# Kernel tuning notes

Measured on AMD Instinct MI355X. Metric: run time of the kernel, lower is better.

Reference implementation:

```python
import jax, jax.numpy as jnp
import numpy as np
import math

HEAD = 4

def _neighbors3x3(t):
    # t: [b, g, d, h, w] -> [b, g, d, 9, h, w], zero-padded 3x3 neighborhoods
    b, g, d, h, w = t.shape
    tp = jnp.pad(t, ((0, 0), (0, 0), (0, 0), (1, 1), (1, 1)))
    # torch.nn.Unfold(kernel_size=3) ordering: kernel positions row-major (dy, dx)
    patches = [tp[:, :, :, dy:dy + h, dx:dx + w] for dy in range(3) for dx in range(3)]
    return jnp.stack(patches, axis=3)


def setup_inputs() -> dict:
    key = jax.random.key(0)
    k1, k2 = jax.random.split(key)
    x = jax.random.normal(k1, (8, 128, 96, 96), dtype=jnp.float32)
    # 1x1 conv weight, no bias: [out=3*out_features, in=in_features]
    W_trans = jax.random.normal(k2, (384, 128), dtype=jnp.float32) * 0.05
    return {"x": x, "W_trans": W_trans}


def reference(x, W_trans):
    b, cin, h, w = x.shape
    # 1x1 conv == channel GEMM
    t = jnp.einsum('bchw,oc->bohw', x, W_trans)  # [b, 3*C, h, w]
    q, k, v = jnp.split(t, 3, axis=1)            # each [b, C, h, w]
    C = q.shape[1]
    d = C // HEAD
    q = q.reshape(b, HEAD, d, h, w)
    k = k.reshape(b, HEAD, d, h, w)
    v = v.reshape(b, HEAD, d, h, w)
    kn = _neighbors3x3(k)  # [b, g, d, 9, h, w]
    vn = _neighbors3x3(v)  # [b, g, d, 9, h, w]
    # att[b,g,n,h,w] = <q[b,g,:,h,w], kn[b,g,:,n,h,w]> / sqrt(d)
    att = jnp.einsum('bgdhw,bgdnhw->bgnhw', q, kn) / math.sqrt(d)
    att = jax.nn.softmax(att, axis=2)
    # dropout p=0.4 is identity in eval mode
    out = jnp.einsum('bgnhw,bgdnhw->bgdhw', att, vn)  # [b, g, d, h, w]
    return out.reshape(b, C, h, w)
```

## Files before the change

### kernel.cpp

```cpp
#include <hip/hip_runtime.h>

#define NB     8
#define CIN    128
#define HEADS  4
#define DHEAD  32
#define HDIM   96
#define WDIM   96
#define HW     9216

#define TH     8
#define TW     16
#define HR     (TH + 2)
#define HC     (TW + 2)
#define HP     (HR * HC)
#define NT     12
#define NPOS   (NT * 16)
#define NPOSP  (NPOS + 1)
#define QP     (TH * TW)

typedef __fp16 f16x2 __attribute__((ext_vector_type(2)));
typedef __fp16 f16x8 __attribute__((ext_vector_type(8)));
typedef float  f32x4 __attribute__((ext_vector_type(4)));

__device__ __forceinline__ unsigned pkh2(float a, float b) {
  f16x2 h = __builtin_amdgcn_cvt_pkrtz(a, b);
  return *(unsigned*)&h;
}
__device__ __forceinline__ float dot2(unsigned a, unsigned b, float c) {
#if __has_builtin(__builtin_amdgcn_fdot2)
  return __builtin_amdgcn_fdot2(*(f16x2*)&a, *(f16x2*)&b, c, false);
#else
  f16x2 ha = *(f16x2*)&a, hb = *(f16x2*)&b;
  c = fmaf((float)ha[0], (float)hb[0], c);
  return fmaf((float)ha[1], (float)hb[1], c);
#endif
}

__global__ __launch_bounds__(256) void wpack_kernel(const float* __restrict__ W,
                                                    uint4* __restrict__ Wf) {
  const int u = blockIdx.x * 256 + threadIdx.x;
  const int lane = u & 63, kb = (u >> 6) & 3, ot = u >> 8;
  const int o = ot * 16 + (lane & 15);
  const int c0 = kb * 32 + (lane >> 4) * 8;
  const float4* w = (const float4*)(W + (size_t)o * CIN + c0);
  float4 w0 = w[0], w1 = w[1];
  uint4 r;
  r.x = pkh2(w0.x, w0.y); r.y = pkh2(w0.z, w0.w);
  r.z = pkh2(w1.x, w1.y); r.w = pkh2(w1.z, w1.w);
  Wf[u] = r;
}

__global__ __launch_bounds__(256) void fused_kernel(const float* __restrict__ x,
                                                    const uint4* __restrict__ Wf,
                                                    float* __restrict__ out) {
  __shared__ uint4 qs[4 * QP];
  __shared__ uint4 ks[4 * NPOSP];
  __shared__ f32x4 vs[8 * NPOSP];

  const int b  = blockIdx.z;
  const int h0 = blockIdx.y * TH;
  const int w0 = blockIdx.x * TW;
  const int t  = threadIdx.x;
  const int wv = t >> 6, lane = t & 63;
  const int colp = lane & 15, quad = lane >> 4;

  uint4 frags[3][4];
  {
    const size_t xbase = (size_t)b * CIN * HW;
#pragma unroll
    for (int i = 0; i < 3; ++i) {
      const int hp = (wv * 3 + i) * 16 + colp;
      const int hr = hp / HC, hc = hp - hr * HC;
      const int hh = h0 - 1 + hr, ww = w0 - 1 + hc;
      const bool ok = (hp < HP) & (hh >= 0) & (hh < HDIM) & (ww >= 0) & (ww < WDIM);
#pragma unroll
      for (int kb = 0; kb < 4; ++kb) {
        const int c0 = kb * 32 + quad * 8;
        float f[8] = {0.f, 0.f, 0.f, 0.f, 0.f, 0.f, 0.f, 0.f};
        if (ok) {
          const size_t pb = xbase + (size_t)(hh * WDIM + ww);
#pragma unroll
          for (int j = 0; j < 8; ++j) f[j] = x[pb + (size_t)(c0 + j) * HW];
        }
        uint4 r;
        r.x = pkh2(f[0], f[1]); r.y = pkh2(f[2], f[3]);
        r.z = pkh2(f[4], f[5]); r.w = pkh2(f[6], f[7]);
        frags[i][kb] = r;
      }
    }
  }

  const int pos = t & 127, dh = t >> 7;
  const int y = pos >> 4, xx = pos & 15;
  const int pbase = (y + 1) * HC + (xx + 1);

#pragma unroll 1
  for (int g = 0; g < 4; ++g) {
    if (g) __syncthreads();

#pragma unroll
    for (int s = 0; s < 3; ++s) {
#pragma unroll
      for (int ph = 0; ph < 2; ++ph) {
        const int ot = s * 8 + g * 2 + ph;
        f16x8 af[4];
#pragma unroll
        for (int kb = 0; kb < 4; ++kb) {
          uint4 tmp = Wf[(ot * 4 + kb) * 64 + lane];
          af[kb] = *(f16x8*)&tmp;
        }
        const int d0 = ph * 16 + quad * 4;
#pragma unroll
        for (int i = 0; i < 3; ++i) {
          f32x4 acc = {0.f, 0.f, 0.f, 0.f};
#pragma unroll
          for (int kb = 0; kb < 4; ++kb)
            acc = __builtin_amdgcn_mfma_f32_16x16x32_f16(
                af[kb], *(f16x8*)&frags[i][kb], acc, 0, 0, 0);
          const int pw = (wv * 3 + i) * 16 + colp;
          if (s == 2) {
            vs[(d0 >> 2) * NPOSP + pw] = acc;
          } else {
            uint2 st;
            st.x = pkh2(acc[0], acc[1]);
            st.y = pkh2(acc[2], acc[3]);
            if (s == 0) {
              const int hr = pw / HC, hc = pw - hr * HC;
              if (((unsigned)(hr - 1) < TH) & ((unsigned)(hc - 1) < TW)) {
                const int idx = (hr - 1) * TW + (hc - 1);
                *(uint2*)((unsigned short*)(qs + (d0 >> 3) * QP + idx)
                          + ((d0 >> 2) & 1) * 4) = st;
              }
            } else {
              *(uint2*)((unsigned short*)(ks + (d0 >> 3) * NPOSP + pw)
                        + ((d0 >> 2) & 1) * 4) = st;
            }
          }
        }
      }
    }
    __syncthreads();

    unsigned qp[16];
#pragma unroll
    for (int c = 0; c < 4; ++c) {
      uint4 u = qs[c * QP + pos];
      qp[c * 4 + 0] = u.x; qp[c * 4 + 1] = u.y;
      qp[c * 4 + 2] = u.z; qp[c * 4 + 3] = u.w;
    }

    float att[9];
#pragma unroll
    for (int nn = 0; nn < 9; ++nn) {
      const int pn = pbase + (nn / 3 - 1) * HC + (nn % 3 - 1);
      float dot = 0.0f;
#pragma unroll
      for (int c = 0; c < 4; ++c) {
        uint4 ku = ks[c * NPOSP + pn];
        dot = dot2(qp[c * 4 + 0], ku.x, dot);
        dot = dot2(qp[c * 4 + 1], ku.y, dot);
        dot = dot2(qp[c * 4 + 2], ku.z, dot);
        dot = dot2(qp[c * 4 + 3], ku.w, dot);
      }
      att[nn] = dot * 0.17677669529663687f;
    }

    float m = att[0];
#pragma unroll
    for (int nn = 1; nn < 9; ++nn) m = fmaxf(m, att[nn]);
    float ssum = 0.0f;
#pragma unroll
    for (int nn = 0; nn < 9; ++nn) { att[nn] = __expf(att[nn] - m); ssum += att[nn]; }
    const float inv = 1.0f / ssum;

    f32x4 acc4[4];
#pragma unroll
    for (int j = 0; j < 4; ++j) acc4[j] = (f32x4){0.f, 0.f, 0.f, 0.f};
#pragma unroll
    for (int nn = 0; nn < 9; ++nn) {
      const float wn = att[nn] * inv;
      const int pn = pbase + (nn / 3 - 1) * HC + (nn % 3 - 1);
#pragma unroll
      for (int j = 0; j < 4; ++j) {
        f32x4 vv = vs[(dh * 4 + j) * NPOSP + pn];
        acc4[j] += wn * vv;
      }
    }

    float* ob = out + ((size_t)b * CIN + (size_t)g * DHEAD + (size_t)dh * 16) * HW
              + (size_t)(h0 + y) * WDIM + (w0 + xx);
#pragma unroll
    for (int j = 0; j < 4; ++j)
#pragma unroll
      for (int e = 0; e < 4; ++e)
        ob[(size_t)(j * 4 + e) * HW] = acc4[j][e];
  }
}

extern "C" void kernel_launch(void* const* d_in, const int* in_sizes, int n_in,
                              void* d_out, int out_size, void* d_ws, size_t ws_size,
                              hipStream_t stream) {
  (void)in_sizes; (void)n_in; (void)out_size; (void)ws_size;
  const float* x = (const float*)d_in[0];
  const float* W = (const float*)d_in[1];
  float* out = (float*)d_out;

  uint4* Wf = (uint4*)d_ws;

  wpack_kernel<<<24, 256, 0, stream>>>(W, Wf);
  fused_kernel<<<dim3(WDIM / TW, HDIM / TH, NB), 256, 0, stream>>>(x, Wf, out);
}
```

Before: 129.9 us.

## Shrink spatial tile to 8x8 and repack weights per head for occupancy

Shrinks the output tile from 8x16 to 8x8, which doubles the block count and cuts per-thread MFMA fragment registers from three position tiles to two (the last wave gets one). Weights are repacked so each head's Q/K/V tiles sit contiguously, and launch bounds request 6 blocks per CU. The attention phase now splits the head dimension into four quarters per position instead of two halves. The trade-off is a larger halo: (10x10)/64 recomputed positions per output pixel versus (10x18)/128, so more x loads and projection MFMAs per output.

```diff
diff --git a/kernel.cpp b/kernel.cpp
--- a/kernel.cpp
+++ b/kernel.cpp
@@ -9,11 +9,11 @@
 #define HW     9216
 
 #define TH     8
-#define TW     16
+#define TW     8
 #define HR     (TH + 2)
 #define HC     (TW + 2)
 #define HP     (HR * HC)
-#define NT     12
+#define NT     7
 #define NPOS   (NT * 16)
 #define NPOSP  (NPOS + 1)
 #define QP     (TH * TW)
@@ -39,20 +39,21 @@
 __global__ __launch_bounds__(256) void wpack_kernel(const float* __restrict__ W,
                                                     uint4* __restrict__ Wf) {
   const int u = blockIdx.x * 256 + threadIdx.x;
-  const int lane = u & 63, kb = (u >> 6) & 3, ot = u >> 8;
-  const int o = ot * 16 + (lane & 15);
+  const int lane = u & 63, kb = (u >> 6) & 3, otp = u >> 8;
+  const int g = otp / 6, r = otp % 6, s = r >> 1, ph = r & 1;
+  const int o = (s * 8 + g * 2 + ph) * 16 + (lane & 15);
   const int c0 = kb * 32 + (lane >> 4) * 8;
   const float4* w = (const float4*)(W + (size_t)o * CIN + c0);
   float4 w0 = w[0], w1 = w[1];
-  uint4 r;
-  r.x = pkh2(w0.x, w0.y); r.y = pkh2(w0.z, w0.w);
-  r.z = pkh2(w1.x, w1.y); r.w = pkh2(w1.z, w1.w);
-  Wf[u] = r;
-}
-
-__global__ __launch_bounds__(256) void fused_kernel(const float* __restrict__ x,
-                                                    const uint4* __restrict__ Wf,
-                                                    float* __restrict__ out) {
+  uint4 rr;
+  rr.x = pkh2(w0.x, w0.y); rr.y = pkh2(w0.z, w0.w);
+  rr.z = pkh2(w1.x, w1.y); rr.w = pkh2(w1.z, w1.w);
+  Wf[u] = rr;
+}
+
+__global__ __launch_bounds__(256, 6) void fused_kernel(const float* __restrict__ x,
+                                                       const uint4* __restrict__ Wf,
+                                                       float* __restrict__ out) {
   __shared__ uint4 qs[4 * QP];
   __shared__ uint4 ks[4 * NPOSP];
   __shared__ f32x4 vs[8 * NPOSP];
@@ -63,35 +64,38 @@
   const int t  = threadIdx.x;
   const int wv = t >> 6, lane = t & 63;
   const int colp = lane & 15, quad = lane >> 4;
-
-  uint4 frags[3][4];
+  const int ntile = (wv == 3) ? 1 : 2;
+
+  uint4 frags[2][4];
   {
     const size_t xbase = (size_t)b * CIN * HW;
 #pragma unroll
-    for (int i = 0; i < 3; ++i) {
-      const int hp = (wv * 3 + i) * 16 + colp;
-      const int hr = hp / HC, hc = hp - hr * HC;
-      const int hh = h0 - 1 + hr, ww = w0 - 1 + hc;
-      const bool ok = (hp < HP) & (hh >= 0) & (hh < HDIM) & (ww >= 0) & (ww < WDIM);
-#pragma unroll
-      for (int kb = 0; kb < 4; ++kb) {
-        const int c0 = kb * 32 + quad * 8;
-        float f[8] = {0.f, 0.f, 0.f, 0.f, 0.f, 0.f, 0.f, 0.f};
-        if (ok) {
-          const size_t pb = xbase + (size_t)(hh * WDIM + ww);
-#pragma unroll
-          for (int j = 0; j < 8; ++j) f[j] = x[pb + (size_t)(c0 + j) * HW];
+    for (int i = 0; i < 2; ++i) {
+      if (i < ntile) {
+        const int hp = (wv * 2 + i) * 16 + colp;
+        const int hr = hp / HC, hc = hp - hr * HC;
+        const int hh = h0 - 1 + hr, ww = w0 - 1 + hc;
+        const bool ok = (hp < HP) & (hh >= 0) & (hh < HDIM) & (ww >= 0) & (ww < WDIM);
+#pragma unroll
+        for (int kb = 0; kb < 4; ++kb) {
+          const int c0 = kb * 32 + quad * 8;
+          float f[8] = {0.f, 0.f, 0.f, 0.f, 0.f, 0.f, 0.f, 0.f};
+          if (ok) {
+            const size_t pb = xbase + (size_t)(hh * WDIM + ww);
+#pragma unroll
+            for (int j = 0; j < 8; ++j) f[j] = x[pb + (size_t)(c0 + j) * HW];
+          }
+          uint4 r;
+          r.x = pkh2(f[0], f[1]); r.y = pkh2(f[2], f[3]);
+          r.z = pkh2(f[4], f[5]); r.w = pkh2(f[6], f[7]);
+          frags[i][kb] = r;
         }
-        uint4 r;
-        r.x = pkh2(f[0], f[1]); r.y = pkh2(f[2], f[3]);
-        r.z = pkh2(f[4], f[5]); r.w = pkh2(f[6], f[7]);
-        frags[i][kb] = r;
       }
     }
   }
 
-  const int pos = t & 127, dh = t >> 7;
-  const int y = pos >> 4, xx = pos & 15;
+  const int pos = t & 63, dq = t >> 6;
+  const int y = pos >> 3, xx = pos & 7;
   const int pbase = (y + 1) * HC + (xx + 1);
 
 #pragma unroll 1
@@ -102,38 +106,40 @@
     for (int s = 0; s < 3; ++s) {
 #pragma unroll
       for (int ph = 0; ph < 2; ++ph) {
-        const int ot = s * 8 + g * 2 + ph;
+        const int otp = g * 6 + s * 2 + ph;
         f16x8 af[4];
 #pragma unroll
         for (int kb = 0; kb < 4; ++kb) {
-          uint4 tmp = Wf[(ot * 4 + kb) * 64 + lane];
+          uint4 tmp = Wf[(otp * 4 + kb) * 64 + lane];
           af[kb] = *(f16x8*)&tmp;
         }
         const int d0 = ph * 16 + quad * 4;
 #pragma unroll
-        for (int i = 0; i < 3; ++i) {
-          f32x4 acc = {0.f, 0.f, 0.f, 0.f};
-#pragma unroll
-          for (int kb = 0; kb < 4; ++kb)
-            acc = __builtin_amdgcn_mfma_f32_16x16x32_f16(
-                af[kb], *(f16x8*)&frags[i][kb], acc, 0, 0, 0);
-          const int pw = (wv * 3 + i) * 16 + colp;
-          if (s == 2) {
-            vs[(d0 >> 2) * NPOSP + pw] = acc;
-          } else {
-            uint2 st;
-            st.x = pkh2(acc[0], acc[1]);
-            st.y = pkh2(acc[2], acc[3]);
-            if (s == 0) {
-              const int hr = pw / HC, hc = pw - hr * HC;
-              if (((unsigned)(hr - 1) < TH) & ((unsigned)(hc - 1) < TW)) {
-                const int idx = (hr - 1) * TW + (hc - 1);
-                *(uint2*)((unsigned short*)(qs + (d0 >> 3) * QP + idx)
+        for (int i = 0; i < 2; ++i) {
+          if (i < ntile) {
+            f32x4 acc = {0.f, 0.f, 0.f, 0.f};
+#pragma unroll
+            for (int kb = 0; kb < 4; ++kb)
+              acc = __builtin_amdgcn_mfma_f32_16x16x32_f16(
+                  af[kb], *(f16x8*)&frags[i][kb], acc, 0, 0, 0);
+            const int pw = (wv * 2 + i) * 16 + colp;
+            if (s == 2) {
+              vs[(d0 >> 2) * NPOSP + pw] = acc;
+            } else {
+              uint2 st;
+              st.x = pkh2(acc[0], acc[1]);
+              st.y = pkh2(acc[2], acc[3]);
+              if (s == 0) {
+                const int hr = pw / HC, hc = pw - hr * HC;
+                if (((unsigned)(hr - 1) < TH) & ((unsigned)(hc - 1) < TW)) {
+                  const int idx = (hr - 1) * TW + (hc - 1);
+                  *(uint2*)((unsigned short*)(qs + (d0 >> 3) * QP + idx)
+                            + ((d0 >> 2) & 1) * 4) = st;
+                }
+              } else {
+                *(uint2*)((unsigned short*)(ks + (d0 >> 3) * NPOSP + pw)
                           + ((d0 >> 2) & 1) * 4) = st;
               }
-            } else {
-              *(uint2*)((unsigned short*)(ks + (d0 >> 3) * NPOSP + pw)
-                        + ((d0 >> 2) & 1) * 4) = st;
             }
           }
         }
@@ -173,24 +179,24 @@
     for (int nn = 0; nn < 9; ++nn) { att[nn] = __expf(att[nn] - m); ssum += att[nn]; }
     const float inv = 1.0f / ssum;
 
-    f32x4 acc4[4];
-#pragma unroll
-    for (int j = 0; j < 4; ++j) acc4[j] = (f32x4){0.f, 0.f, 0.f, 0.f};
+    f32x4 acc4[2];
+#pragma unroll
+    for (int j = 0; j < 2; ++j) acc4[j] = (f32x4){0.f, 0.f, 0.f, 0.f};
 #pragma unroll
     for (int nn = 0; nn < 9; ++nn) {
       const float wn = att[nn] * inv;
       const int pn = pbase + (nn / 3 - 1) * HC + (nn % 3 - 1);
 #pragma unroll
-      for (int j = 0; j < 4; ++j) {
-        f32x4 vv = vs[(dh * 4 + j) * NPOSP + pn];
+      for (int j = 0; j < 2; ++j) {
+        f32x4 vv = vs[(dq * 2 + j) * NPOSP + pn];
         acc4[j] += wn * vv;
       }
     }
 
-    float* ob = out + ((size_t)b * CIN + (size_t)g * DHEAD + (size_t)dh * 16) * HW
+    float* ob = out + ((size_t)b * CIN + (size_t)g * DHEAD + (size_t)dq * 8) * HW
               + (size_t)(h0 + y) * WDIM + (w0 + xx);
 #pragma unroll
-    for (int j = 0; j < 4; ++j)
+    for (int j = 0; j < 2; ++j)
 #pragma unroll
       for (int e = 0; e < 4; ++e)
         ob[(size_t)(j * 4 + e) * HW] = acc4[j][e];
```

Result: slower. 169.9 us (+30.8%).

## Pre-pack x to fp16 channel-last, split heads across blocks, store V in fp16

Applied to the files above, without the earlier changes.

Adds a pre-pass kernel that converts x to fp16 in a position-major, channel-contiguous layout, so the fused kernel loads each fragment with one 16-byte read instead of eight strided fp32 loads. The fused grid is doubled so each block handles two of the four heads, with the weight pack reordered to match, giving more parallelism and higher occupancy via launch bounds. V is now kept in LDS as fp16 rather than fp32, halving its shared memory footprint. In exchange the x halo is re-read by two blocks, the extra pass writes and re-reads an fp16 copy of x, and V loses precision.

```diff
diff --git a/kernel.cpp b/kernel.cpp
--- a/kernel.cpp
+++ b/kernel.cpp
@@ -36,28 +36,60 @@
 #endif
 }
 
+__global__ __launch_bounds__(256) void xpack_kernel(const float* __restrict__ x,
+                                                    uint4* __restrict__ xT) {
+  __shared__ unsigned l[64 * 67];
+  const int b  = blockIdx.y;
+  const int p0 = blockIdx.x * 64;
+  const int t  = threadIdx.x;
+  const int p  = t & 63, cg = t >> 6;
+  const float* xb = x + (size_t)b * CIN * HW + p0 + p;
+#pragma unroll
+  for (int i = 0; i < 16; ++i) {
+    const int c = cg * 32 + 2 * i;
+    float f0 = xb[(size_t)c * HW];
+    float f1 = xb[(size_t)(c + 1) * HW];
+    l[p * 67 + cg * 16 + i] = pkh2(f0, f1);
+  }
+  __syncthreads();
+  uint4* dst = xT + ((size_t)b * HW + p0) * 16;
+#pragma unroll
+  for (int k = 0; k < 4; ++k) {
+    const int u = k * 256 + t;
+    const int pos = u >> 4, ch = u & 15;
+    uint4 d;
+    d.x = l[pos * 67 + ch * 4 + 0];
+    d.y = l[pos * 67 + ch * 4 + 1];
+    d.z = l[pos * 67 + ch * 4 + 2];
+    d.w = l[pos * 67 + ch * 4 + 3];
+    dst[u] = d;
+  }
+}
+
 __global__ __launch_bounds__(256) void wpack_kernel(const float* __restrict__ W,
                                                     uint4* __restrict__ Wf) {
   const int u = blockIdx.x * 256 + threadIdx.x;
-  const int lane = u & 63, kb = (u >> 6) & 3, ot = u >> 8;
-  const int o = ot * 16 + (lane & 15);
+  const int lane = u & 63, kb = (u >> 6) & 3, otp = u >> 8;
+  const int g = otp / 6, r = otp % 6, s = r >> 1, ph = r & 1;
+  const int o = (s * 8 + g * 2 + ph) * 16 + (lane & 15);
   const int c0 = kb * 32 + (lane >> 4) * 8;
   const float4* w = (const float4*)(W + (size_t)o * CIN + c0);
   float4 w0 = w[0], w1 = w[1];
-  uint4 r;
-  r.x = pkh2(w0.x, w0.y); r.y = pkh2(w0.z, w0.w);
-  r.z = pkh2(w1.x, w1.y); r.w = pkh2(w1.z, w1.w);
-  Wf[u] = r;
-}
-
-__global__ __launch_bounds__(256) void fused_kernel(const float* __restrict__ x,
-                                                    const uint4* __restrict__ Wf,
-                                                    float* __restrict__ out) {
+  uint4 rr;
+  rr.x = pkh2(w0.x, w0.y); rr.y = pkh2(w0.z, w0.w);
+  rr.z = pkh2(w1.x, w1.y); rr.w = pkh2(w1.z, w1.w);
+  Wf[u] = rr;
+}
+
+__global__ __launch_bounds__(256, 4) void fused_kernel(const uint4* __restrict__ xT,
+                                                       const uint4* __restrict__ Wf,
+                                                       float* __restrict__ out) {
   __shared__ uint4 qs[4 * QP];
   __shared__ uint4 ks[4 * NPOSP];
-  __shared__ f32x4 vs[8 * NPOSP];
-
-  const int b  = blockIdx.z;
+  __shared__ uint4 vs[4 * NPOSP];
+
+  const int z  = blockIdx.z;
+  const int b  = z >> 1, hpair = z & 1;
   const int h0 = blockIdx.y * TH;
   const int w0 = blockIdx.x * TW;
   const int t  = threadIdx.x;
@@ -66,7 +98,7 @@
 
   uint4 frags[3][4];
   {
-    const size_t xbase = (size_t)b * CIN * HW;
+    const size_t xb16 = (size_t)b * HW * 16;
 #pragma unroll
     for (int i = 0; i < 3; ++i) {
       const int hp = (wv * 3 + i) * 16 + colp;
@@ -75,16 +107,9 @@
       const bool ok = (hp < HP) & (hh >= 0) & (hh < HDIM) & (ww >= 0) & (ww < WDIM);
 #pragma unroll
       for (int kb = 0; kb < 4; ++kb) {
-        const int c0 = kb * 32 + quad * 8;
-        float f[8] = {0.f, 0.f, 0.f, 0.f, 0.f, 0.f, 0.f, 0.f};
-        if (ok) {
-          const size_t pb = xbase + (size_t)(hh * WDIM + ww);
-#pragma unroll
-          for (int j = 0; j < 8; ++j) f[j] = x[pb + (size_t)(c0 + j) * HW];
-        }
-        uint4 r;
-        r.x = pkh2(f[0], f[1]); r.y = pkh2(f[2], f[3]);
-        r.z = pkh2(f[4], f[5]); r.w = pkh2(f[6], f[7]);
+        uint4 r = {0u, 0u, 0u, 0u};
+        if (ok)
+          r = xT[xb16 + (size_t)(hh * WDIM + ww) * 16 + kb * 4 + quad];
         frags[i][kb] = r;
       }
     }
@@ -95,18 +120,19 @@
   const int pbase = (y + 1) * HC + (xx + 1);
 
 #pragma unroll 1
-  for (int g = 0; g < 4; ++g) {
-    if (g) __syncthreads();
+  for (int gi = 0; gi < 2; ++gi) {
+    const int g = hpair * 2 + gi;
+    if (gi) __syncthreads();
 
 #pragma unroll
     for (int s = 0; s < 3; ++s) {
 #pragma unroll
       for (int ph = 0; ph < 2; ++ph) {
-        const int ot = s * 8 + g * 2 + ph;
+        const int otp = g * 6 + s * 2 + ph;
         f16x8 af[4];
 #pragma unroll
         for (int kb = 0; kb < 4; ++kb) {
-          uint4 tmp = Wf[(ot * 4 + kb) * 64 + lane];
+          uint4 tmp = Wf[(otp * 4 + kb) * 64 + lane];
           af[kb] = *(f16x8*)&tmp;
         }
         const int d0 = ph * 16 + quad * 4;
@@ -118,23 +144,20 @@
             acc = __builtin_amdgcn_mfma_f32_16x16x32_f16(
                 af[kb], *(f16x8*)&frags[i][kb], acc, 0, 0, 0);
           const int pw = (wv * 3 + i) * 16 + colp;
-          if (s == 2) {
-            vs[(d0 >> 2) * NPOSP + pw] = acc;
-          } else {
-            uint2 st;
-            st.x = pkh2(acc[0], acc[1]);
-            st.y = pkh2(acc[2], acc[3]);
-            if (s == 0) {
-              const int hr = pw / HC, hc = pw - hr * HC;
-              if (((unsigned)(hr - 1) < TH) & ((unsigned)(hc - 1) < TW)) {
-                const int idx = (hr - 1) * TW + (hc - 1);
-                *(uint2*)((unsigned short*)(qs + (d0 >> 3) * QP + idx)
-                          + ((d0 >> 2) & 1) * 4) = st;
-              }
-            } else {
-              *(uint2*)((unsigned short*)(ks + (d0 >> 3) * NPOSP + pw)
+          uint2 st;
+          st.x = pkh2(acc[0], acc[1]);
+          st.y = pkh2(acc[2], acc[3]);
+          if (s == 0) {
+            const int hr = pw / HC, hc = pw - hr * HC;
+            if (((unsigned)(hr - 1) < TH) & ((unsigned)(hc - 1) < TW)) {
+              const int idx = (hr - 1) * TW + (hc - 1);
+              *(uint2*)((unsigned short*)(qs + (d0 >> 3) * QP + idx)
                         + ((d0 >> 2) & 1) * 4) = st;
             }
+          } else {
+            uint4* dst = (s == 1) ? ks : vs;
+            *(uint2*)((unsigned short*)(dst + (d0 >> 3) * NPOSP + pw)
+                      + ((d0 >> 2) & 1) * 4) = st;
           }
         }
       }
@@ -173,27 +196,33 @@
     for (int nn = 0; nn < 9; ++nn) { att[nn] = __expf(att[nn] - m); ssum += att[nn]; }
     const float inv = 1.0f / ssum;
 
-    f32x4 acc4[4];
-#pragma unroll
-    for (int j = 0; j < 4; ++j) acc4[j] = (f32x4){0.f, 0.f, 0.f, 0.f};
+    float acc[16];
+#pragma unroll
+    for (int i = 0; i < 16; ++i) acc[i] = 0.0f;
 #pragma unroll
     for (int nn = 0; nn < 9; ++nn) {
       const float wn = att[nn] * inv;
       const int pn = pbase + (nn / 3 - 1) * HC + (nn % 3 - 1);
 #pragma unroll
-      for (int j = 0; j < 4; ++j) {
-        f32x4 vv = vs[(dh * 4 + j) * NPOSP + pn];
-        acc4[j] += wn * vv;
+      for (int cc = 0; cc < 2; ++cc) {
+        uint4 vv = vs[(dh * 2 + cc) * NPOSP + pn];
+        f16x2 h0 = *(f16x2*)&vv.x, h1 = *(f16x2*)&vv.y;
+        f16x2 h2 = *(f16x2*)&vv.z, h3 = *(f16x2*)&vv.w;
+        acc[cc * 8 + 0] = fmaf(wn, (float)h0[0], acc[cc * 8 + 0]);
+        acc[cc * 8 + 1] = fmaf(wn, (float)h0[1], acc[cc * 8 + 1]);
+        acc[cc * 8 + 2] = fmaf(wn, (float)h1[0], acc[cc * 8 + 2]);
+        acc[cc * 8 + 3] = fmaf(wn, (float)h1[1], acc[cc * 8 + 3]);
+        acc[cc * 8 + 4] = fmaf(wn, (float)h2[0], acc[cc * 8 + 4]);
+        acc[cc * 8 + 5] = fmaf(wn, (float)h2[1], acc[cc * 8 + 5]);
+        acc[cc * 8 + 6] = fmaf(wn, (float)h3[0], acc[cc * 8 + 6]);
+        acc[cc * 8 + 7] = fmaf(wn, (float)h3[1], acc[cc * 8 + 7]);
       }
     }
 
     float* ob = out + ((size_t)b * CIN + (size_t)g * DHEAD + (size_t)dh * 16) * HW
               + (size_t)(h0 + y) * WDIM + (w0 + xx);
 #pragma unroll
-    for (int j = 0; j < 4; ++j)
-#pragma unroll
-      for (int e = 0; e < 4; ++e)
-        ob[(size_t)(j * 4 + e) * HW] = acc4[j][e];
+    for (int i = 0; i < 16; ++i) ob[(size_t)i * HW] = acc[i];
   }
 }
 
@@ -205,8 +234,10 @@
   const float* W = (const float*)d_in[1];
   float* out = (float*)d_out;
 
-  uint4* Wf = (uint4*)d_ws;
-
+  uint4* xT = (uint4*)d_ws;
+  uint4* Wf = (uint4*)((char*)d_ws + (size_t)NB * HW * 256);
+
+  xpack_kernel<<<dim3(HW / 64, NB), 256, 0, stream>>>(x, xT);
   wpack_kernel<<<24, 256, 0, stream>>>(W, Wf);
-  fused_kernel<<<dim3(WDIM / TW, HDIM / TH, NB), 256, 0, stream>>>(x, Wf, out);
-}
+  fused_kernel<<<dim3(WDIM / TW, HDIM / TH, NB * 2), 256, 0, stream>>>(xT, Wf, out);
+}
```

Result: faster. 119.8 us (-7.8%).
